# Kernel optimization log

Measured on AMD Instinct MI355X. Metric: run time of the kernel, lower is better.

The kernel has to match this reference:

```python
import jax, jax.numpy as jnp
import numpy as np

B, T, E, H = 2, 256, 256, 4
LN_EPS = 1e-5
W_SCALE = 0.05  # keep softmax logits in a sane range


def _heads(x):
    # [B,T,E*H] -> [B,T,E,H]; torch chunk(H,-1)+stack(-1) puts EH index h*E+d at [...,d,h]
    b, t, eh = x.shape
    return jnp.swapaxes(x.reshape(b, t, H, eh // H), -1, -2)


def setup_inputs() -> dict:
    key = jax.random.key(0)
    k = jax.random.split(key, 6)
    return {
        "position_embeddings": jax.random.normal(k[0], (B, T, E), dtype=jnp.float32),
        "values": jax.random.normal(k[1], (B, T, E), dtype=jnp.float32),
        "ln_w": jnp.ones((E,), dtype=jnp.float32),
        "ln_b": jnp.zeros((E,), dtype=jnp.float32),
        "Wq": jax.random.normal(k[2], (E * H, E), dtype=jnp.float32) * W_SCALE,
        "Wk": jax.random.normal(k[3], (E * H, E), dtype=jnp.float32) * W_SCALE,
        "Wv": jax.random.normal(k[4], (E * H, E), dtype=jnp.float32) * W_SCALE,
        "Wp": jax.random.normal(k[5], (E, E * H), dtype=jnp.float32) * W_SCALE,
    }


def reference(position_embeddings, values, ln_w, ln_b, Wq, Wk, Wv, Wp):
    # LayerNorm over last dim
    mu = jnp.mean(position_embeddings, axis=-1, keepdims=True)
    var = jnp.var(position_embeddings, axis=-1, keepdims=True)
    x = (position_embeddings - mu) * jax.lax.rsqrt(var + LN_EPS) * ln_w + ln_b

    Qh = _heads(x @ Wq.T)        # [B,T,E,H]
    Kh = _heads(x @ Wk.T)        # [B,T,E,H]
    Vh = _heads(values @ Wv.T)   # [B,T,E,H]

    # elementwise Q-K difference: [B,T(query t),T(key w),E,H]
    S = Qh[:, :, None, :, :] - Kh[:, None, :, :, :]
    A = jax.nn.softmax(S, axis=2)  # softmax over w (dim -3)

    # outputs[b,t,d,h] = V[b,t,d,h] * sum_w A[b,t,w,d,h]
    out = jnp.einsum('btdh,btwdh->btdh', Vh, A)

    # flatten(-2): [B,T,E,H] -> [B,T,E*H] with index d*H+h, then project
    return out.reshape(B, T, E * H) @ Wp.T
```

## Files before the change

### kernel.cpp

```cpp
#include <hip/hip_runtime.h>


constexpr int E  = 256;
constexpr int H  = 4;
constexpr int EH = E * H;
constexpr int BT = 512;

__global__ __launch_bounds__(1024) void build_m_kernel(
    const float* __restrict__ Wv, const float* __restrict__ Wp,
    float* __restrict__ MT)
{
    const int tid  = threadIdx.x;
    const int lane = tid & 63;
    const int kc   = tid >> 6;
    const int dsub = lane >> 4;
    const int jq   = lane & 15;
    const int i0   = (blockIdx.x >> 2) * 4;
    const int j0   = (blockIdx.x & 3) * 64;

    __shared__ float sWp[4][EH];
    ((float4*)sWp)[tid] = ((const float4*)(Wp + i0 * EH))[tid];
    __syncthreads();

    const int dbase = kc * 16 + dsub * 4;
    const int jj    = j0 + jq * 4;

    float4 a0 = {0,0,0,0}, a1 = {0,0,0,0}, a2 = {0,0,0,0}, a3 = {0,0,0,0};
    #pragma unroll
    for (int h = 0; h < H; ++h) {
        const float* __restrict__ p = Wv + (h * E + dbase) * E + jj;
        #pragma unroll
        for (int it = 0; it < 4; ++it) {
            const float4 wv = *(const float4*)(p + it * E);
            const int    k  = (dbase + it) * 4 + h;
            const float w0 = sWp[0][k], w1 = sWp[1][k];
            const float w2 = sWp[2][k], w3 = sWp[3][k];
            a0.x += w0*wv.x; a0.y += w0*wv.y; a0.z += w0*wv.z; a0.w += w0*wv.w;
            a1.x += w1*wv.x; a1.y += w1*wv.y; a1.z += w1*wv.z; a1.w += w1*wv.w;
            a2.x += w2*wv.x; a2.y += w2*wv.y; a2.z += w2*wv.z; a2.w += w2*wv.w;
            a3.x += w3*wv.x; a3.y += w3*wv.y; a3.z += w3*wv.z; a3.w += w3*wv.w;
        }
    }

    #pragma unroll
    for (int mask = 16; mask < 64; mask <<= 1) {
        a0.x += __shfl_xor(a0.x, mask); a0.y += __shfl_xor(a0.y, mask);
        a0.z += __shfl_xor(a0.z, mask); a0.w += __shfl_xor(a0.w, mask);
        a1.x += __shfl_xor(a1.x, mask); a1.y += __shfl_xor(a1.y, mask);
        a1.z += __shfl_xor(a1.z, mask); a1.w += __shfl_xor(a1.w, mask);
        a2.x += __shfl_xor(a2.x, mask); a2.y += __shfl_xor(a2.y, mask);
        a2.z += __shfl_xor(a2.z, mask); a2.w += __shfl_xor(a2.w, mask);
        a3.x += __shfl_xor(a3.x, mask); a3.y += __shfl_xor(a3.y, mask);
        a3.z += __shfl_xor(a3.z, mask); a3.w += __shfl_xor(a3.w, mask);
    }

    __shared__ float sAcc[16][4][64];
    if (lane < 16) {
        *(float4*)&sAcc[kc][0][jq * 4] = a0;
        *(float4*)&sAcc[kc][1][jq * 4] = a1;
        *(float4*)&sAcc[kc][2][jq * 4] = a2;
        *(float4*)&sAcc[kc][3][jq * 4] = a3;
    }
    __syncthreads();

    if (tid < 256) {
        const int ii = tid & 3, jl = tid >> 2;
        float v = 0.f;
        #pragma unroll
        for (int c = 0; c < 16; ++c) v += sAcc[c][ii][jl];
        MT[(j0 + jl) * E + i0 + ii] = v;
    }
}

__global__ __launch_bounds__(1024) void apply_kernel(
    const float* __restrict__ values, const float* __restrict__ MT,
    float* __restrict__ out)
{
    const int tid = threadIdx.x;
    const int e0  = (tid & 63) * 4;
    const int rr  = (tid >> 6) & 1;
    const int jc  = tid >> 7;
    const int r0  = blockIdx.x * 2;

    __shared__ float sv[2][E];
    if (tid < 2 * E) sv[tid >> 8][tid & 255] = values[r0 * E + tid];
    __syncthreads();

    float4 acc = {0,0,0,0};
    #pragma unroll
    for (int jj = 0; jj < 32; ++jj) {
        const int    j = jc * 32 + jj;
        const float4 m = *(const float4*)&MT[j * E + e0];
        const float  s = sv[rr][j];
        acc.x += s * m.x; acc.y += s * m.y; acc.z += s * m.z; acc.w += s * m.w;
    }

    __shared__ float sAc2[8][2][E];
    *(float4*)&sAc2[jc][rr][e0] = acc;
    __syncthreads();

    if (tid < 2 * E) {
        const int r_idx = tid >> 8, e = tid & 255;
        float v = 0.f;
        #pragma unroll
        for (int c = 0; c < 8; ++c) v += sAc2[c][r_idx][e];
        out[(r0 + r_idx) * E + e] = v;
    }
}

extern "C" void kernel_launch(void* const* d_in, const int* in_sizes, int n_in,
                              void* d_out, int out_size, void* d_ws, size_t ws_size,
                              hipStream_t stream) {
    const float* values = (const float*)d_in[1];
    const float* Wv     = (const float*)d_in[6];
    const float* Wp     = (const float*)d_in[7];
    float*       out    = (float*)d_out;
    float*       MT     = (float*)d_ws;

    build_m_kernel<<<256, 1024, 0, stream>>>(Wv, Wp, MT);
    apply_kernel<<<BT / 2, 1024, 0, stream>>>(values, MT, out);
}
```

Measured before the change: 79.34 us.

## Retile weight-fold and apply kernels for more blocks and MT reuse

The weight-combining kernel is split across twice as many blocks, each handling a narrower column slab, to raise parallelism. The apply kernel now processes 8 token rows over a 64-wide output slice per block, so each loaded MT vector feeds two rows and the total MT traffic per block drops. Partial sums are reduced through a padded shared buffer. This adds shuffle steps and more complex indexing in exchange for less global/L2 traffic.

```diff
diff --git a/kernel.cpp b/kernel.cpp
--- a/kernel.cpp
+++ b/kernel.cpp
@@ -4,7 +4,6 @@
 constexpr int E  = 256;
 constexpr int H  = 4;
 constexpr int EH = E * H;
-constexpr int BT = 512;
 
 __global__ __launch_bounds__(1024) void build_m_kernel(
     const float* __restrict__ Wv, const float* __restrict__ Wp,
@@ -13,16 +12,16 @@
     const int tid  = threadIdx.x;
     const int lane = tid & 63;
     const int kc   = tid >> 6;
-    const int dsub = lane >> 4;
-    const int jq   = lane & 15;
-    const int i0   = (blockIdx.x >> 2) * 4;
-    const int j0   = (blockIdx.x & 3) * 64;
+    const int dsub = lane >> 3;
+    const int jq   = lane & 7;
+    const int i0   = (blockIdx.x >> 3) * 4;
+    const int j0   = (blockIdx.x & 7) * 32;
 
     __shared__ float sWp[4][EH];
     ((float4*)sWp)[tid] = ((const float4*)(Wp + i0 * EH))[tid];
     __syncthreads();
 
-    const int dbase = kc * 16 + dsub * 4;
+    const int dbase = (kc * 8 + dsub) * 2;
     const int jj    = j0 + jq * 4;
 
     float4 a0 = {0,0,0,0}, a1 = {0,0,0,0}, a2 = {0,0,0,0}, a3 = {0,0,0,0};
@@ -30,7 +29,7 @@
     for (int h = 0; h < H; ++h) {
         const float* __restrict__ p = Wv + (h * E + dbase) * E + jj;
         #pragma unroll
-        for (int it = 0; it < 4; ++it) {
+        for (int it = 0; it < 2; ++it) {
             const float4 wv = *(const float4*)(p + it * E);
             const int    k  = (dbase + it) * 4 + h;
             const float w0 = sWp[0][k], w1 = sWp[1][k];
@@ -43,7 +42,7 @@
     }
 
     #pragma unroll
-    for (int mask = 16; mask < 64; mask <<= 1) {
+    for (int mask = 8; mask < 64; mask <<= 1) {
         a0.x += __shfl_xor(a0.x, mask); a0.y += __shfl_xor(a0.y, mask);
         a0.z += __shfl_xor(a0.z, mask); a0.w += __shfl_xor(a0.w, mask);
         a1.x += __shfl_xor(a1.x, mask); a1.y += __shfl_xor(a1.y, mask);
@@ -54,8 +53,8 @@
         a3.z += __shfl_xor(a3.z, mask); a3.w += __shfl_xor(a3.w, mask);
     }
 
-    __shared__ float sAcc[16][4][64];
-    if (lane < 16) {
+    __shared__ float sAcc[16][4][36];
+    if (dsub == 0) {
         *(float4*)&sAcc[kc][0][jq * 4] = a0;
         *(float4*)&sAcc[kc][1][jq * 4] = a1;
         *(float4*)&sAcc[kc][2][jq * 4] = a2;
@@ -63,7 +62,7 @@
     }
     __syncthreads();
 
-    if (tid < 256) {
+    if (tid < 128) {
         const int ii = tid & 3, jl = tid >> 2;
         float v = 0.f;
         #pragma unroll
@@ -76,35 +75,52 @@
     const float* __restrict__ values, const float* __restrict__ MT,
     float* __restrict__ out)
 {
-    const int tid = threadIdx.x;
-    const int e0  = (tid & 63) * 4;
-    const int rr  = (tid >> 6) & 1;
-    const int jc  = tid >> 7;
-    const int r0  = blockIdx.x * 2;
+    const int tid  = threadIdx.x;
+    const int lane = tid & 63;
+    const int kc   = tid >> 6;
+    const int dsub = lane >> 4;
+    const int el   = lane & 15;
+    const int r0   = (blockIdx.x >> 2) * 8;
+    const int eb   = (blockIdx.x & 3) * 64;
+    const int e0   = eb + el * 4;
 
-    __shared__ float sv[2][E];
-    if (tid < 2 * E) sv[tid >> 8][tid & 255] = values[r0 * E + tid];
+    __shared__ float sV[8][257];
+    {
+        const int f0 = tid;
+        sV[f0 >> 8][f0 & 255] = values[(r0 + (f0 >> 8)) * E + (f0 & 255)];
+        const int f1 = tid + 1024;
+        sV[f1 >> 8][f1 & 255] = values[(r0 + (f1 >> 8)) * E + (f1 & 255)];
+    }
     __syncthreads();
 
-    float4 acc = {0,0,0,0};
+    float4 acc0 = {0,0,0,0}, acc1 = {0,0,0,0};
     #pragma unroll
-    for (int jj = 0; jj < 32; ++jj) {
-        const int    j = jc * 32 + jj;
+    for (int jjj = 0; jjj < 16; ++jjj) {
+        const int    j = kc * 16 + jjj;
         const float4 m = *(const float4*)&MT[j * E + e0];
-        const float  s = sv[rr][j];
-        acc.x += s * m.x; acc.y += s * m.y; acc.z += s * m.z; acc.w += s * m.w;
+        const float v0 = sV[dsub * 2 + 0][j];
+        const float v1 = sV[dsub * 2 + 1][j];
+        acc0.x += v0*m.x; acc0.y += v0*m.y; acc0.z += v0*m.z; acc0.w += v0*m.w;
+        acc1.x += v1*m.x; acc1.y += v1*m.y; acc1.z += v1*m.z; acc1.w += v1*m.w;
     }
 
-    __shared__ float sAc2[8][2][E];
-    *(float4*)&sAc2[jc][rr][e0] = acc;
+    __shared__ float sP[16][4][16][9];
+    #pragma unroll
+    for (int c = 0; c < 4; ++c) {
+        sP[kc][dsub][el][c]     = (&acc0.x)[c];
+        sP[kc][dsub][el][4 + c] = (&acc1.x)[c];
+    }
     __syncthreads();
 
-    if (tid < 2 * E) {
-        const int r_idx = tid >> 8, e = tid & 255;
+    if (tid < 512) {
+        const int r   = tid >> 6;
+        const int e_l = tid & 63;
+        const int ds2 = r >> 1, ri = r & 1;
+        const int el2 = e_l >> 2, c = e_l & 3;
         float v = 0.f;
         #pragma unroll
-        for (int c = 0; c < 8; ++c) v += sAc2[c][r_idx][e];
-        out[(r0 + r_idx) * E + e] = v;
+        for (int k = 0; k < 16; ++k) v += sP[k][ds2][el2][ri * 4 + c];
+        out[(r0 + r) * E + eb + e_l] = v;
     }
 }
 
@@ -117,6 +133,6 @@
     float*       out    = (float*)d_out;
     float*       MT     = (float*)d_ws;
 
-    build_m_kernel<<<256, 1024, 0, stream>>>(Wv, Wp, MT);
-    apply_kernel<<<BT / 2, 1024, 0, stream>>>(values, MT, out);
+    build_m_kernel<<<512, 1024, 0, stream>>>(Wv, Wp, MT);
+    apply_kernel<<<256, 1024, 0, stream>>>(values, MT, out);
 }
```

After: 80.70 us. No clear change (+1.7%).
